# Kernel optimization log

Hardware: AMD Instinct MI355X
Metric: run time of the kernel (lower is better)

The kernel has to match this reference:

```python
import jax, jax.numpy as jnp
import numpy as np

N = 128       # HiPPO order
BATCH = 2
L = 2048      # max_length / sequence length
GBT_ALPHA = 0.5
STEP = 1.0


def _legs_transition(n_order):
    """HiPPO-LegS transition matrices A (N,N), B (N,1) as in TransMatrix(measure='legs')."""
    q = np.arange(n_order, dtype=np.float64)
    col, row = np.meshgrid(q, q)
    r = 2 * q + 1
    M = -(np.where(row >= col, r, 0.0) - np.diag(q))   # lower-tri + diag
    T = np.sqrt(2 * q + 1)
    A = (T[:, None] * M) / T[None, :]                  # T @ M @ inv(T)
    B = T[:, None]
    return A.astype(np.float32), B.astype(np.float32)


def setup_inputs() -> dict:
    key = jax.random.key(0)
    f = jax.random.normal(key, (BATCH, L, 1), dtype=jnp.float32)
    A_np, B_np = _legs_transition(N)
    return {
        "f": f,
        "A": jnp.asarray(A_np),
        "B": jnp.asarray(B_np),
        "C": jnp.ones((N, 1), dtype=jnp.float32),
        "D": jnp.zeros((1,), dtype=jnp.float32),
    }


def _discretize(A, B, step, alpha):
    """Generalized bilinear transform (alpha=0.5 -> bilinear)."""
    I = jnp.eye(A.shape[0], dtype=A.dtype)
    ss = 1.0 / step
    p1 = I - ss * alpha * A
    Ad = jnp.linalg.solve(p1, I + ss * (1.0 - alpha) * A)
    Bd = jnp.linalg.solve(p1, ss * B)
    return Ad, Bd


def reference(f, A, B, C, D):
    """HiPPO lti recurrence (verbose=False): returns (c_final, y_seq).
    c_final: (batch, 1, N); y_seq: (batch, L, N, N)."""
    n = A.shape[0]
    Ad, Bd = _discretize(A, B, STEP, GBT_ALPHA)          # (N,N), (N,1)
    c0 = jnp.zeros((f.shape[0], 1, n), dtype=f.dtype)     # init_state default
    f_t_first = jnp.swapaxes(f, 0, 1)                     # (L, batch, 1)

    def step(c, f_t):
        # c: (batch, 1, N), f_t: (batch, 1)
        c_new = c @ Ad.T + Bd.T * f_t[:, :, None]         # (batch, 1, N)
        # faithful to source: y_k = C @ c_k + D * f_k  ->  outer product (N,N)
        y = jnp.einsum('nm,bmk->bnk', C, c_new) + (D * f_t)[:, :, None]
        return c_new, y

    c_fin, ys = jax.lax.scan(step, c0, f_t_first)         # ys: (L, batch, N, N)
    ys = jnp.swapaxes(ys, 0, 1)                           # (batch, L, N, N)
    return c_fin, ys
```

## Files before the change

kernel.cpp:

```cpp
#include <hip/hip_runtime.h>
#include <math.h>

#define NSTATE 128
#define LSEQ   2048
#define NBATCH 2

typedef float f32x4 __attribute__((ext_vector_type(4)));

#define WS_AD   0
#define WS_BD   16384
#define WS_MB0  16512
#define WS_V    49280
#define WS_PART 311424

__global__ void k_init(float* __restrict__ Ad, float* __restrict__ Bd,
                       float* __restrict__ V) {
    __shared__ double u[128], invd[128];
    int j = threadIdx.x;
    if (j < 128) { u[j] = sqrt(2.0 * j + 1.0); invd[j] = 1.0 / (1.0 + 0.5 * (j + 1)); }
    __syncthreads();
    if (j > 128) return;
    double S = 0.0;
    double uj = (j < 128) ? u[j] : 0.0;
    for (int i = 0; i < 128; ++i) {
        double ui = u[i];
        double b;
        if (j == 128)      b = ui;
        else if (i < j)    b = 0.0;
        else if (i == j)   b = 1.0 - 0.5 * (j + 1);
        else               b = -0.5 * ui * uj;
        double x = (b - 0.5 * ui * S) * invd[i];
        S += ui * x;
        if (j == 128) { Bd[i] = (float)x; V[i] = (float)x; }
        else Ad[i * 128 + j] = (float)x;
    }
}

__device__ __forceinline__ void chain_run(const float4 a[8], float4 vr[8],
                                          float* __restrict__ vb,
                                          int n, int h, int steps,
                                          float* __restrict__ Vst, int vstride,
                                          float* __restrict__ Mst) {
    for (int s = 1; s <= steps; ++s) {
        float s0 = 0.f, s1 = 0.f, s2 = 0.f, s3 = 0.f;
        #pragma unroll
        for (int q = 0; q < 8; ++q) {
            s0 = fmaf(a[q].x, vr[q].x, s0);
            s1 = fmaf(a[q].y, vr[q].y, s1);
            s2 = fmaf(a[q].z, vr[q].z, s2);
            s3 = fmaf(a[q].w, vr[q].w, s3);
        }
        float p = (s0 + s1) + (s2 + s3);
        p += __shfl_xor(p, 1);
        p += __shfl_xor(p, 2);
        float* cur = vb + (s & 1) * 144;
        if (h == 0) {
            cur[36 * (n >> 5) + (n & 31)] = p;
            if (Vst) Vst[s * vstride + n] = p;
            if (Mst && s == steps) Mst[n * 128] = p;
        }
        __syncthreads();
        const float4* vv = (const float4*)(cur + 36 * h);
        #pragma unroll
        for (int q = 0; q < 8; ++q) vr[q] = vv[q];
    }
}

__global__ __launch_bounds__(512) void k_pow(const float* __restrict__ Ad,
                                             const float* __restrict__ Bd,
                                             float* __restrict__ V,
                                             float* __restrict__ M) {
    int blk = blockIdx.x, tid = threadIdx.x;
    int n = tid >> 2, h = tid & 3;
    __shared__ float vb[2 * 144];
    float4 a[8];
    const float4* Ar = (const float4*)(Ad + n * 128 + 32 * h);
    #pragma unroll
    for (int q = 0; q < 8; ++q) a[q] = Ar[q];
    float4 vr[8];
    if (blk == 128) {
        const float4* Bv = (const float4*)(Bd + 32 * h);
        #pragma unroll
        for (int q = 0; q < 8; ++q) vr[q] = Bv[q];
        chain_run(a, vr, vb, n, h, 31, V, 128, nullptr);
    } else {
        #pragma unroll
        for (int q = 0; q < 8; ++q) {
            vr[q].x = (32 * h + 4 * q + 0 == blk) ? 1.f : 0.f;
            vr[q].y = (32 * h + 4 * q + 1 == blk) ? 1.f : 0.f;
            vr[q].z = (32 * h + 4 * q + 2 == blk) ? 1.f : 0.f;
            vr[q].w = (32 * h + 4 * q + 3 == blk) ? 1.f : 0.f;
        }
        chain_run(a, vr, vb, n, h, 32, nullptr, 0, M + blk);
    }
}

__global__ __launch_bounds__(512) void k_starts(const float* __restrict__ M,
                                                const float* __restrict__ Bd,
                                                float* __restrict__ V) {
    int tid = threadIdx.x;
    int n = tid >> 2, h = tid & 3;
    __shared__ float vb[2 * 144];
    float4 a[8];
    const float4* Ar = (const float4*)(M + n * 128 + 32 * h);
    #pragma unroll
    for (int q = 0; q < 8; ++q) a[q] = Ar[q];
    float4 vr[8];
    const float4* Bv = (const float4*)(Bd + 32 * h);
    #pragma unroll
    for (int q = 0; q < 8; ++q) vr[q] = Bv[q];
    chain_run(a, vr, vb, n, h, 63, V, 32 * 128, nullptr);
}

__global__ __launch_bounds__(512) void k_tails(const float* __restrict__ Ad,
                                               float* __restrict__ V) {
    int c = blockIdx.x + 1, tid = threadIdx.x;
    int n = tid >> 2, h = tid & 3;
    __shared__ float vb[2 * 144];
    float4 a[8];
    const float4* Ar = (const float4*)(Ad + n * 128 + 32 * h);
    #pragma unroll
    for (int q = 0; q < 8; ++q) a[q] = Ar[q];
    float4 vr[8];
    float* Vrow = V + (size_t)c * 32 * 128;
    const float4* Sv = (const float4*)(Vrow + 32 * h);
    #pragma unroll
    for (int q = 0; q < 8; ++q) vr[q] = Sv[q];
    chain_run(a, vr, vb, n, h, 31, Vrow, 128, nullptr);
}

__global__ __launch_bounds__(512) void k_conv(const float* __restrict__ f,
                                              const float* __restrict__ V,
                                              float* __restrict__ part) {
    int b = blockIdx.x, tile = blockIdx.y, z = blockIdx.z;
    int t0 = tile * 128, d0 = z * 256;
    if (d0 > t0 + 127) return;
    __shared__ float fL[384];
    int tid = threadIdx.x;
    int base = t0 - d0 - 255;
    if (tid < 384) {
        int g = base + tid;
        fL[tid] = (g >= 0 && g < LSEQ) ? f[b * LSEQ + g] : 0.f;
    }
    __syncthreads();
    int k = tid & 127, h = tid >> 7;
    float acc[32];
    #pragma unroll
    for (int i = 0; i < 32; ++i) acc[i] = 0.f;
    for (int dbl = 0; dbl < 16; ++dbl) {
        int offF = 240 + 32 * h - 16 * dbl;
        float F[48];
        const float4* fv = (const float4*)(fL + offF);
        #pragma unroll
        for (int q = 0; q < 12; ++q) {
            float4 t4 = fv[q];
            F[4 * q] = t4.x; F[4 * q + 1] = t4.y; F[4 * q + 2] = t4.z; F[4 * q + 3] = t4.w;
        }
        int dbase = d0 + dbl * 16;
        #pragma unroll
        for (int dd = 0; dd < 16; ++dd) {
            float w = V[(dbase + dd) * 128 + k];
            #pragma unroll
            for (int i = 0; i < 32; ++i) acc[i] += w * F[15 + i - dd];
        }
    }
    float* oc = part + (((size_t)z * NBATCH + b) * LSEQ + t0) * 128;
    #pragma unroll
    for (int i = 0; i < 32; ++i) oc[(32 * h + i) * 128 + k] = acc[i];
}

__global__ __launch_bounds__(256) void k_write(const float* __restrict__ part,
                                               float* __restrict__ out) {
    int bt = blockIdx.x;
    int b = bt >> 11, t = bt & 2047;
    int tile = t >> 7;
    int nz = (tile >> 1) + 1;
    int tid = threadIdx.x;
    int k4 = (tid & 31) * 4;
    f32x4 v = {0.f, 0.f, 0.f, 0.f};
    for (int z = 0; z < nz; ++z)
        v += *(const f32x4*)(part + (((size_t)z * NBATCH + b) * LSEQ + t) * 128 + k4);
    float* ys = out + 256 + (size_t)(b * LSEQ + t) * 16384;
    int n0 = tid >> 5;
    #pragma unroll
    for (int it = 0; it < 16; ++it) {
        int n = n0 + 8 * it;
        __builtin_nontemporal_store(v, (f32x4*)(ys + n * 128 + k4));
    }
    if (t == LSEQ - 1 && tid < 32) *(f32x4*)(out + b * 128 + k4) = v;
}

extern "C" void kernel_launch(void* const* d_in, const int* in_sizes, int n_in,
                              void* d_out, int out_size, void* d_ws, size_t ws_size,
                              hipStream_t stream) {
    const float* f = (const float*)d_in[0];
    float* ws   = (float*)d_ws;
    float* Ad   = ws + WS_AD;
    float* Bd   = ws + WS_BD;
    float* M32  = ws + WS_MB0;
    float* V    = ws + WS_V;
    float* part = ws + WS_PART;
    float* out  = (float*)d_out;

    k_init  <<<1,   256, 0, stream>>>(Ad, Bd, V);
    k_pow   <<<129, 512, 0, stream>>>(Ad, Bd, V, M32);
    k_starts<<<1,   512, 0, stream>>>(M32, Bd, V);
    k_tails <<<63,  512, 0, stream>>>(Ad, V);
    dim3 cgrid(2, 16, 8);
    k_conv  <<<cgrid, 512, 0, stream>>>(f, V, part);
    k_write <<<4096, 256, 0, stream>>>(part, out);
}
```

Baseline: 375.9 us.

## Fuse convolution and broadcast write into one kernel with in-block reduction

Replaces the two-stage convolution, which wrote partial sums per delay chunk to workspace, and the separate write kernel that summed them and broadcast them, with one kernel. Each block handles 8 timesteps across all delays, splits the delay range across 4 thread groups, reduces them in shared memory and writes the 128x128 broadcast output directly. This removes the partial-sum round trip through global memory and one launch. The cost is uneven per-block work, since later tiles cover many more delays, and re-reading V for every 8-timestep tile.

New measurement: 340.4 us. 9.4% less time.

```diff
diff --git a/kernel.cpp b/kernel.cpp
--- a/kernel.cpp
+++ b/kernel.cpp
@@ -11,7 +11,6 @@
 #define WS_BD   16384
 #define WS_MB0  16512
 #define WS_V    49280
-#define WS_PART 311424
 
 __global__ void k_init(float* __restrict__ Ad, float* __restrict__ Bd,
                        float* __restrict__ V) {
@@ -129,65 +128,72 @@
     chain_run(a, vr, vb, n, h, 31, Vrow, 128, nullptr);
 }
 
-__global__ __launch_bounds__(512) void k_conv(const float* __restrict__ f,
-                                              const float* __restrict__ V,
-                                              float* __restrict__ part) {
-    int b = blockIdx.x, tile = blockIdx.y, z = blockIdx.z;
-    int t0 = tile * 128, d0 = z * 256;
-    if (d0 > t0 + 127) return;
-    __shared__ float fL[384];
+__global__ __launch_bounds__(512) void k_convwrite(const float* __restrict__ f,
+                                                   const float* __restrict__ V,
+                                                   float* __restrict__ out) {
+    int b = blockIdx.x, tile = blockIdx.y;
+    int t0 = tile * 8;
+    int Dtot = t0 + 8;
+    __shared__ float fL[2080];
+    __shared__ float red[4][8][128];
     int tid = threadIdx.x;
-    int base = t0 - d0 - 255;
-    if (tid < 384) {
-        int g = base + tid;
-        fL[tid] = (g >= 0 && g < LSEQ) ? f[b * LSEQ + g] : 0.f;
-    }
-    __syncthreads();
+    if (tid < 15) fL[tid] = 0.f;
+    for (int x = tid; x < Dtot; x += 512) fL[15 + x] = f[b * LSEQ + x];
+    __syncthreads();
+
     int k = tid & 127, h = tid >> 7;
-    float acc[32];
-    #pragma unroll
-    for (int i = 0; i < 32; ++i) acc[i] = 0.f;
-    for (int dbl = 0; dbl < 16; ++dbl) {
-        int offF = 240 + 32 * h - 16 * dbl;
-        float F[48];
-        const float4* fv = (const float4*)(fL + offF);
-        #pragma unroll
-        for (int q = 0; q < 12; ++q) {
-            float4 t4 = fv[q];
+    float acc[8];
+    #pragma unroll
+    for (int i = 0; i < 8; ++i) acc[i] = 0.f;
+
+    int nblk = (Dtot + 15) >> 4;
+    for (int ib = h; ib < nblk; ib += 4) {
+        int dbase = ib << 4;
+        int foff = t0 - dbase;
+        float F[24];
+        const f32x4* fv = (const f32x4*)(fL + foff);
+        #pragma unroll
+        for (int q = 0; q < 6; ++q) {
+            f32x4 t4 = fv[q];
             F[4 * q] = t4.x; F[4 * q + 1] = t4.y; F[4 * q + 2] = t4.z; F[4 * q + 3] = t4.w;
         }
-        int dbase = d0 + dbl * 16;
+        const float* Vp = V + (size_t)dbase * 128 + k;
         #pragma unroll
         for (int dd = 0; dd < 16; ++dd) {
-            float w = V[(dbase + dd) * 128 + k];
+            float w = Vp[dd * 128];
             #pragma unroll
-            for (int i = 0; i < 32; ++i) acc[i] += w * F[15 + i - dd];
-        }
-    }
-    float* oc = part + (((size_t)z * NBATCH + b) * LSEQ + t0) * 128;
-    #pragma unroll
-    for (int i = 0; i < 32; ++i) oc[(32 * h + i) * 128 + k] = acc[i];
-}
-
-__global__ __launch_bounds__(256) void k_write(const float* __restrict__ part,
-                                               float* __restrict__ out) {
-    int bt = blockIdx.x;
-    int b = bt >> 11, t = bt & 2047;
-    int tile = t >> 7;
-    int nz = (tile >> 1) + 1;
-    int tid = threadIdx.x;
-    int k4 = (tid & 31) * 4;
-    f32x4 v = {0.f, 0.f, 0.f, 0.f};
-    for (int z = 0; z < nz; ++z)
-        v += *(const f32x4*)(part + (((size_t)z * NBATCH + b) * LSEQ + t) * 128 + k4);
-    float* ys = out + 256 + (size_t)(b * LSEQ + t) * 16384;
-    int n0 = tid >> 5;
-    #pragma unroll
-    for (int it = 0; it < 16; ++it) {
-        int n = n0 + 8 * it;
-        __builtin_nontemporal_store(v, (f32x4*)(ys + n * 128 + k4));
-    }
-    if (t == LSEQ - 1 && tid < 32) *(f32x4*)(out + b * 128 + k4) = v;
+            for (int i = 0; i < 8; ++i)
+                acc[i] = fmaf(w, F[15 + i - dd], acc[i]);
+        }
+    }
+
+    #pragma unroll
+    for (int i = 0; i < 8; ++i) red[h][i][k] = acc[i];
+    __syncthreads();
+    if (tid < 128) {
+        #pragma unroll
+        for (int i = 0; i < 8; ++i) {
+            float s = red[0][i][tid] + red[1][i][tid] + red[2][i][tid] + red[3][i][tid];
+            red[0][i][tid] = s;
+        }
+    }
+    __syncthreads();
+
+    const f32x4* outv = (const f32x4*)&red[0][0][0];
+    int k32 = tid & 31, r0 = tid >> 5;
+    float* ysb = out + 256 + ((size_t)(b * LSEQ + t0)) * 16384;
+    #pragma unroll
+    for (int t = 0; t < 8; ++t) {
+        f32x4 v = outv[t * 32 + k32];
+        float* yst = ysb + (size_t)t * 16384 + k32 * 4;
+        #pragma unroll
+        for (int p = 0; p < 8; ++p) {
+            int n = p * 16 + r0;
+            __builtin_nontemporal_store(v, (f32x4*)(yst + n * 128));
+        }
+    }
+    if (tile == 255 && tid < 32)
+        *(f32x4*)(out + b * 128 + tid * 4) = outv[7 * 32 + tid];
 }
 
 extern "C" void kernel_launch(void* const* d_in, const int* in_sizes, int n_in,
@@ -199,14 +205,12 @@
     float* Bd   = ws + WS_BD;
     float* M32  = ws + WS_MB0;
     float* V    = ws + WS_V;
-    float* part = ws + WS_PART;
     float* out  = (float*)d_out;
 
     k_init  <<<1,   256, 0, stream>>>(Ad, Bd, V);
     k_pow   <<<129, 512, 0, stream>>>(Ad, Bd, V, M32);
     k_starts<<<1,   512, 0, stream>>>(M32, Bd, V);
     k_tails <<<63,  512, 0, stream>>>(Ad, V);
-    dim3 cgrid(2, 16, 8);
-    k_conv  <<<cgrid, 512, 0, stream>>>(f, V, part);
-    k_write <<<4096, 256, 0, stream>>>(part, out);
-}
+    dim3 cw(2, 256);
+    k_convwrite<<<cw, 512, 0, stream>>>(f, V, out);
+}
```
